# Performance work log

Hardware: AMD Instinct MI355X
Metric: run time of the kernel (lower is better)

The kernel has to match this reference:

```python
import jax, jax.numpy as jnp
import numpy as np

B, T, V, C, K = 256, 2048, 128, 512, 10


def setup_inputs() -> dict:
    key = jax.random.key(0)
    k0, k1, k2, k3 = jax.random.split(key, 4)
    x = jax.random.normal(k0, (B, C), dtype=jnp.float32)
    # kappa_old: running attention position, non-negative, somewhere in [0, T)
    kappa_old = jax.random.uniform(k1, (B, K), dtype=jnp.float32) * T
    # onehots: one-hot encoded text, (B, T, V)
    char_ids = jax.random.randint(k2, (B, T), 0, V)
    onehots = jax.nn.one_hot(char_ids, V, dtype=jnp.float32)
    # Linear(cell_size, 3*K) params; torch stores weight as (out, in)
    W = jax.random.normal(k3, (3 * K, C), dtype=jnp.float32) * 0.02
    b = jnp.zeros((3 * K,), dtype=jnp.float32)
    return {"x": x, "kappa_old": kappa_old, "onehots": onehots, "W": W, "b": b}


def reference(x, kappa_old, onehots, W, b):
    max_text_len = onehots.shape[1]
    params = jnp.exp(x @ W.T + b)                      # (B, 3K)
    alpha, beta, pre_kappa = jnp.split(params, 3, axis=-1)  # each (B, K)
    kappa = kappa_old + pre_kappa                      # (B, K)
    indices = jnp.arange(max_text_len, dtype=x.dtype)  # (T,)
    # gravity: (B, K, T) via broadcast, then exp + alpha-weighted reduce over K
    gravity = -beta[:, :, None] * (kappa[:, :, None] - indices) ** 2
    phi = jnp.einsum("bk,bkt->bt", alpha, jnp.exp(gravity))  # (B, T)
    w = jnp.einsum("bt,btv->bv", phi, onehots)               # (B, V)
    return (w, kappa, phi)
```

## Files before the change

kernel.cpp:

```cpp
#include <hip/hip_runtime.h>

#define B_ 256
#define T_ 2048
#define V_ 128
#define C_ 512
#define K_ 10

#define W_OFF 0
#define KAPPA_OFF (B_ * V_)
#define PHI_OFF   (B_ * V_ + B_ * K_)

__global__ __launch_bounds__(256) void phi_kernel(
    const float* __restrict__ x, const float* __restrict__ kappa_old,
    const float* __restrict__ W, const float* __restrict__ bias,
    float* __restrict__ out) {
  const int b = blockIdx.x;
  const int tid = threadIdx.x;

  __shared__ float xs[C_];
  __shared__ float alpha_s[K_];
  __shared__ float beta_s[K_];
  __shared__ float kap_s[K_];

  xs[tid]       = x[b * C_ + tid];
  xs[tid + 256] = x[b * C_ + tid + 256];
  if (tid < V_) out[W_OFF + b * V_ + tid] = 0.0f;
  __syncthreads();

  const int j = tid >> 3;
  const int l = tid & 7;
  if (j < 3 * K_) {
    const float* Wr = W + j * C_;
    float acc = 0.0f;
#pragma unroll 8
    for (int i = l; i < C_; i += 8) acc = fmaf(xs[i], Wr[i], acc);
    acc += __shfl_down(acc, 4, 8);
    acc += __shfl_down(acc, 2, 8);
    acc += __shfl_down(acc, 1, 8);
    if (l == 0) {
      float p = expf(acc + bias[j]);
      if (j < K_) {
        alpha_s[j] = p;
      } else if (j < 2 * K_) {
        beta_s[j - K_] = p;
      } else {
        float kk = kappa_old[b * K_ + (j - 2 * K_)] + p;
        kap_s[j - 2 * K_] = kk;
        out[KAPPA_OFF + b * K_ + (j - 2 * K_)] = kk;
      }
    }
  }
  __syncthreads();

  for (int t = tid; t < T_; t += 256) {
    const float ft = (float)t;
    float s = 0.0f;
#pragma unroll
    for (int k = 0; k < K_; k++) {
      const float d = kap_s[k] - ft;
      s += alpha_s[k] * expf(-beta_s[k] * d * d);
    }
    out[PHI_OFF + b * T_ + t] = s;
  }
}

#define S_ 8
#define TS_ (T_ / S_)

__global__ __launch_bounds__(256) void wsum_kernel(
    const float* __restrict__ onehots, float* __restrict__ out) {
  const int s = blockIdx.x;
  const int b = blockIdx.y;
  const int tid = threadIdx.x;

  __shared__ float phs[TS_];
  phs[tid] = out[PHI_OFF + b * T_ + s * TS_ + tid];
  __syncthreads();

  const int vg = tid & 31;
  const int tr = tid >> 5;
  const float4* base =
      (const float4*)(onehots + ((size_t)b * T_ + (size_t)s * TS_) * V_);

  float4 acc = make_float4(0.f, 0.f, 0.f, 0.f);
#pragma unroll 4
  for (int t = tr; t < TS_; t += 8) {
    const float p = phs[t];
    const float4 o = base[t * (V_ / 4) + vg];
    acc.x = fmaf(p, o.x, acc.x);
    acc.y = fmaf(p, o.y, acc.y);
    acc.z = fmaf(p, o.z, acc.z);
    acc.w = fmaf(p, o.w, acc.w);
  }

  __shared__ float red[8 * V_];
  *(float4*)&red[tr * V_ + vg * 4] = acc;
  __syncthreads();

  if (tid < V_) {
    float s0 = 0.0f;
#pragma unroll
    for (int r = 0; r < 8; r++) s0 += red[r * V_ + tid];
    atomicAdd(&out[W_OFF + b * V_ + tid], s0);
  }
}

extern "C" void kernel_launch(void* const* d_in, const int* in_sizes, int n_in,
                              void* d_out, int out_size, void* d_ws,
                              size_t ws_size, hipStream_t stream) {
  const float* x         = (const float*)d_in[0];
  const float* kappa_old = (const float*)d_in[1];
  const float* onehots   = (const float*)d_in[2];
  const float* W         = (const float*)d_in[3];
  const float* bias      = (const float*)d_in[4];
  float* out = (float*)d_out;

  phi_kernel<<<dim3(B_), dim3(256), 0, stream>>>(x, kappa_old, W, bias, out);
  wsum_kernel<<<dim3(S_, B_), dim3(256), 0, stream>>>(onehots, out);
}
```

Measured before the change: 371.9 us.

## Fuse phi computation and onehot weighted sum into one kernel

Merges the phi kernel and the w-reduction kernel into a single launch where each (slice, batch) block recomputes the small linear projection, computes its phi slice into shared memory, and reduces the onehots slice directly. This removes the phi round trip through global memory and one kernel launch, and raises parallelism for phi computation from B blocks to S*B blocks. The projection is now done redundantly 8 times per batch row, and the output is zeroed by a memset. It also vectorizes the W dot product, switches to fast __expf, and increases the unroll factor.

```diff
diff --git a/kernel.cpp b/kernel.cpp
--- a/kernel.cpp
+++ b/kernel.cpp
@@ -10,71 +10,72 @@
 #define KAPPA_OFF (B_ * V_)
 #define PHI_OFF   (B_ * V_ + B_ * K_)
 
-__global__ __launch_bounds__(256) void phi_kernel(
+#define S_ 8
+#define TS_ (T_ / S_)
+
+__global__ __launch_bounds__(256) void window_fused(
     const float* __restrict__ x, const float* __restrict__ kappa_old,
     const float* __restrict__ W, const float* __restrict__ bias,
-    float* __restrict__ out) {
-  const int b = blockIdx.x;
+    const float* __restrict__ onehots, float* __restrict__ out) {
+  const int s = blockIdx.x;
+  const int b = blockIdx.y;
   const int tid = threadIdx.x;
 
-  __shared__ float xs[C_];
+  __shared__ float4 xs4[C_ / 4];
   __shared__ float alpha_s[K_];
   __shared__ float beta_s[K_];
   __shared__ float kap_s[K_];
+  __shared__ float phs[TS_];
 
-  xs[tid]       = x[b * C_ + tid];
-  xs[tid + 256] = x[b * C_ + tid + 256];
-  if (tid < V_) out[W_OFF + b * V_ + tid] = 0.0f;
+  if (tid < C_ / 4) xs4[tid] = ((const float4*)(x + b * C_))[tid];
   __syncthreads();
 
   const int j = tid >> 3;
   const int l = tid & 7;
   if (j < 3 * K_) {
-    const float* Wr = W + j * C_;
-    float acc = 0.0f;
-#pragma unroll 8
-    for (int i = l; i < C_; i += 8) acc = fmaf(xs[i], Wr[i], acc);
+    const float4* Wr = (const float4*)(W + j * C_);
+    float4 a4 = make_float4(0.f, 0.f, 0.f, 0.f);
+#pragma unroll
+    for (int m = 0; m < 16; ++m) {
+      const float4 wv = Wr[m * 8 + l];
+      const float4 xv = xs4[m * 8 + l];
+      a4.x = fmaf(wv.x, xv.x, a4.x);
+      a4.y = fmaf(wv.y, xv.y, a4.y);
+      a4.z = fmaf(wv.z, xv.z, a4.z);
+      a4.w = fmaf(wv.w, xv.w, a4.w);
+    }
+    float acc = (a4.x + a4.y) + (a4.z + a4.w);
     acc += __shfl_down(acc, 4, 8);
     acc += __shfl_down(acc, 2, 8);
     acc += __shfl_down(acc, 1, 8);
     if (l == 0) {
-      float p = expf(acc + bias[j]);
+      const float p = __expf(acc + bias[j]);
       if (j < K_) {
         alpha_s[j] = p;
       } else if (j < 2 * K_) {
         beta_s[j - K_] = p;
       } else {
-        float kk = kappa_old[b * K_ + (j - 2 * K_)] + p;
-        kap_s[j - 2 * K_] = kk;
-        out[KAPPA_OFF + b * K_ + (j - 2 * K_)] = kk;
+        const int k = j - 2 * K_;
+        const float kk = kappa_old[b * K_ + k] + p;
+        kap_s[k] = kk;
+        if (s == 0) out[KAPPA_OFF + b * K_ + k] = kk;
       }
     }
   }
   __syncthreads();
 
-  for (int t = tid; t < T_; t += 256) {
+  {
+    const int t = s * TS_ + tid;
     const float ft = (float)t;
-    float s = 0.0f;
+    float ph = 0.0f;
 #pragma unroll
     for (int k = 0; k < K_; k++) {
       const float d = kap_s[k] - ft;
-      s += alpha_s[k] * expf(-beta_s[k] * d * d);
+      ph += alpha_s[k] * __expf(-beta_s[k] * d * d);
     }
-    out[PHI_OFF + b * T_ + t] = s;
+    phs[tid] = ph;
+    out[PHI_OFF + b * T_ + t] = ph;
   }
-}
-
-#define S_ 8
-#define TS_ (T_ / S_)
-
-__global__ __launch_bounds__(256) void wsum_kernel(
-    const float* __restrict__ onehots, float* __restrict__ out) {
-  const int s = blockIdx.x;
-  const int b = blockIdx.y;
-  const int tid = threadIdx.x;
-
-  __shared__ float phs[TS_];
-  phs[tid] = out[PHI_OFF + b * T_ + s * TS_ + tid];
   __syncthreads();
 
   const int vg = tid & 31;
@@ -83,7 +84,7 @@
       (const float4*)(onehots + ((size_t)b * T_ + (size_t)s * TS_) * V_);
 
   float4 acc = make_float4(0.f, 0.f, 0.f, 0.f);
-#pragma unroll 4
+#pragma unroll 8
   for (int t = tr; t < TS_; t += 8) {
     const float p = phs[t];
     const float4 o = base[t * (V_ / 4) + vg];
@@ -115,6 +116,7 @@
   const float* bias      = (const float*)d_in[4];
   float* out = (float*)d_out;
 
-  phi_kernel<<<dim3(B_), dim3(256), 0, stream>>>(x, kappa_old, W, bias, out);
-  wsum_kernel<<<dim3(S_, B_), dim3(256), 0, stream>>>(onehots, out);
+  hipMemsetAsync(d_out, 0, B_ * V_ * sizeof(float), stream);
+  window_fused<<<dim3(S_, B_), dim3(256), 0, stream>>>(x, kappa_old, W, bias,
+                                                       onehots, out);
 }
```

New measurement: 368.2 us. Within noise of the previous version (-1.0%).
